# Performance work log

Measured on AMD Instinct MI355X. Metric: run time of the kernel, lower is better.

Reference implementation:

```python
import jax, jax.numpy as jnp
import numpy as np

N, E = 100000, 1600000
D_IN, H, C = 128, 4, 32
NEG_SLOPE = 0.2

def setup_inputs() -> dict:
    key = jax.random.key(0)
    ks = jax.random.split(key, 6)
    x = jax.random.normal(ks[0], (N, D_IN), dtype=jnp.float32)
    edge_index = jax.random.randint(ks[1], (2, E), 0, N, dtype=jnp.int64)
    s = 1.0 / np.sqrt(D_IN)
    W_l = jax.random.normal(ks[2], (D_IN, H * C), dtype=jnp.float32) * s
    W_r = jax.random.normal(ks[3], (D_IN, H * C), dtype=jnp.float32) * s
    att = jax.random.normal(ks[4], (H, C), dtype=jnp.float32) * (1.0 / np.sqrt(C))
    bias = jax.random.normal(ks[5], (H * C,), dtype=jnp.float32) * 0.01
    return {"x": x, "edge_index": edge_index, "W_l": W_l, "W_r": W_r, "att": att, "bias": bias}

def reference(x, edge_index, W_l, W_r, att, bias):
    # GATv2: e_ij = att . LeakyReLU(W_l x_j + W_r x_i); softmax over incoming edges of i;
    # out_i = sum_j alpha_ij * (W_l x_j); heads concatenated, then bias.
    src, dst = edge_index[0], edge_index[1]
    n = x.shape[0]
    xl = (x @ W_l).reshape(n, H, C)   # source transform (lin_l)
    xr = (x @ W_r).reshape(n, H, C)   # target transform (lin_r)
    xj = xl[src]                       # [E,H,C] gathered source feats
    xi = xr[dst]                       # [E,H,C] gathered target feats
    e = jax.nn.leaky_relu(xi + xj, NEG_SLOPE)
    score = jnp.einsum('ehc,hc->eh', e, att)          # [E,H]
    # segment softmax over destination nodes
    m = jax.ops.segment_max(score, dst, num_segments=n)  # [N,H]
    ex = jnp.exp(score - m[dst])
    denom = jax.ops.segment_sum(ex, dst, num_segments=n)  # [N,H]
    alpha = ex / (denom[dst] + 1e-16)                      # [E,H]
    out = jax.ops.segment_sum(alpha[..., None] * xj, dst, num_segments=n)  # [N,H,C]
    return out.reshape(n, H * C) + bias
```

## Files before the change

kernel.cpp:

```cpp
#include <hip/hip_runtime.h>
#include <hip/hip_bf16.h>
#include <math.h>

#define N_NODES 100000
#define E_EDGES 1600000
#define D 128
#define NEG_SLOPE 0.2f

#define BSH   8
#define NBKT  391
#define BCAP  4992
#define P1_EPB 8192

typedef __bf16 bf16x8 __attribute__((ext_vector_type(8)));
typedef float f32x4 __attribute__((ext_vector_type(4)));

__device__ __forceinline__ float bf2f(unsigned short u) {
    union { unsigned int i; float f; } x; x.i = ((unsigned int)u) << 16; return x.f;
}
__device__ __forceinline__ unsigned short f2bf(float f) {
    union { float f; unsigned int i; } x; x.f = f;
    unsigned int r = x.i + 0x7fffu + ((x.i >> 16) & 1u);
    return (unsigned short)(r >> 16);
}
__device__ __forceinline__ void unpack4(uint2 u, float* x) {
    union { unsigned int i; float f; } a, b, c, d;
    a.i = u.x << 16; b.i = u.x & 0xffff0000u;
    c.i = u.y << 16; d.i = u.y & 0xffff0000u;
    x[0] = a.f; x[1] = b.f; x[2] = c.f; x[3] = d.f;
}

__global__ void GATv2Conv_56908316672629_kernel(
    const unsigned int* ei_words, int* flags)
{
    __shared__ int cnt_edge;
    if (threadIdx.x == 0) cnt_edge = 0;
    __syncthreads();
    unsigned int w = ei_words[2 * threadIdx.x + 1];
    if (w != 0u) atomicAdd(&cnt_edge, 1);
    __syncthreads();
    if (threadIdx.x == 0) flags[0] = (cnt_edge == 0) ? 1 : 0;
}

__global__ __launch_bounds__(256) void gemm_f32_kernel(
    const float* __restrict__ X,
    const float* __restrict__ Wl,
    const float* __restrict__ Wr,
    unsigned short* __restrict__ xl, unsigned short* __restrict__ xr,
    int nblk)
{
    __shared__ unsigned short Xs[64][136];
    __shared__ unsigned short Wt[128][136];

    const int bid = blockIdx.x;
    const int sel = (bid >= nblk) ? 1 : 0;
    const float* W = sel ? Wr : Wl;
    unsigned short* out = sel ? xr : xl;
    const int rowbase = (bid - sel * nblk) * 64;
    const int tid = threadIdx.x;

    for (int c = tid; c < 4096; c += 256) {
        int k = c >> 5, n4 = (c & 31) << 2;
        float4 w = ((const float4*)(W + (size_t)k * D))[c & 31];
        Wt[n4 + 0][k] = f2bf(w.x);
        Wt[n4 + 1][k] = f2bf(w.y);
        Wt[n4 + 2][k] = f2bf(w.z);
        Wt[n4 + 3][k] = f2bf(w.w);
    }
    for (int c = tid; c < 2048; c += 256) {
        int r = c >> 5, k4 = (c & 31) << 2;
        int grow = rowbase + r;
        float4 v = make_float4(0.f, 0.f, 0.f, 0.f);
        if (grow < N_NODES) v = ((const float4*)(X + (size_t)grow * D))[c & 31];
        union { unsigned short us[4]; uint2 u2; } pk;
        pk.us[0] = f2bf(v.x); pk.us[1] = f2bf(v.y);
        pk.us[2] = f2bf(v.z); pk.us[3] = f2bf(v.w);
        *((uint2*)&Xs[r][k4]) = pk.u2;
    }
    __syncthreads();

    const int wave = tid >> 6, lane = tid & 63;
    const int mrow = lane & 15, quad = lane >> 4;

    f32x4 acc[8];
#pragma unroll
    for (int i = 0; i < 8; ++i) acc[i] = (f32x4){0.f, 0.f, 0.f, 0.f};

#pragma unroll
    for (int kk = 0; kk < 4; ++kk) {
        const int k0 = kk * 32 + quad * 8;
        bf16x8 afrag = *(const bf16x8*)&Xs[wave * 16 + mrow][k0];
#pragma unroll
        for (int n0 = 0; n0 < 8; ++n0) {
            bf16x8 bfrag = *(const bf16x8*)&Wt[n0 * 16 + mrow][k0];
            acc[n0] = __builtin_amdgcn_mfma_f32_16x16x32_bf16(afrag, bfrag, acc[n0], 0, 0, 0);
        }
    }

    const int grow0 = rowbase + wave * 16 + quad * 4;
#pragma unroll
    for (int n0 = 0; n0 < 8; ++n0) {
        int col = n0 * 16 + mrow;
#pragma unroll
        for (int r = 0; r < 4; ++r) {
            int grow = grow0 + r;
            if (grow < N_NODES) out[(size_t)grow * D + col] = f2bf(acc[n0][r]);
        }
    }
}

__global__ void zero_kernel(int* p, int n) {
    int i = blockIdx.x * 256 + threadIdx.x;
    if (i < n) p[i] = 0;
}

__device__ __forceinline__ unsigned int edge_word(const unsigned int* ei, int is64,
                                                  long long entry) {
    return is64 ? ei[2 * entry] : ei[entry];
}

__global__ __launch_bounds__(256) void bucket_scatter_kernel(
    const unsigned int* __restrict__ ei, const int* __restrict__ flags,
    int* __restrict__ bcur, unsigned int* __restrict__ pairbuf)
{
    __shared__ int h[NBKT];
    __shared__ int gbase[NBKT];

    const int tid = threadIdx.x;
    const int is64 = flags[0];
    const long long e0 = (long long)blockIdx.x * P1_EPB;
    int n = E_EDGES - (int)e0; if (n > P1_EPB) n = P1_EPB;

    for (int i = tid; i < NBKT; i += 256) h[i] = 0;
    __syncthreads();

    for (int i = tid; i < n; i += 256) {
        unsigned int s = edge_word(ei, is64, e0 + i);
        unsigned int d = edge_word(ei, is64, (long long)E_EDGES + e0 + i);
        if (d < N_NODES && s < N_NODES) atomicAdd(&h[d >> BSH], 1);
    }
    __syncthreads();

    for (int i = tid; i < NBKT; i += 256) {
        int c = h[i];
        gbase[i] = c ? atomicAdd(&bcur[i], c) : 0;
        h[i] = 0;
    }
    __syncthreads();

    for (int i = tid; i < n; i += 256) {
        unsigned int s = edge_word(ei, is64, e0 + i);
        unsigned int d = edge_word(ei, is64, (long long)E_EDGES + e0 + i);
        if (d < N_NODES && s < N_NODES) {
            int b = (int)(d >> BSH);
            int r = gbase[b] + atomicAdd(&h[b], 1);
            if (r < BCAP)
                pairbuf[(size_t)b * BCAP + r] = s | ((d & 255u) << 24);
        }
    }
}

__global__ __launch_bounds__(256) void bucket_sort_kernel(
    const int* __restrict__ bcur, unsigned int* __restrict__ pairbuf,
    int* __restrict__ rowstart, int* __restrict__ rowend)
{
    __shared__ unsigned int stage[BCAP];
    __shared__ int cnt[256];
    __shared__ int base[256];

    const int b = blockIdx.x;
    const int tid = threadIdx.x;
    int n = bcur[b]; if (n > BCAP) n = BCAP;
    unsigned int* buf = pairbuf + (size_t)b * BCAP;

    for (int i = tid; i < n; i += 256) stage[i] = buf[i];
    cnt[tid] = 0;
    __syncthreads();

    for (int i = tid; i < n; i += 256) atomicAdd(&cnt[stage[i] >> 24], 1);
    __syncthreads();

    int v = cnt[tid];
    base[tid] = v;
    __syncthreads();
    for (int off = 1; off < 256; off <<= 1) {
        int u = (tid >= off) ? base[tid - off] : 0;
        __syncthreads();
        base[tid] += u;
        __syncthreads();
    }
    const int myend = base[tid];
    const int mystart = myend - v;

    const int node = b * 256 + tid;
    if (node < N_NODES) {
        rowstart[node] = b * BCAP + mystart;
        rowend[node]   = b * BCAP + myend;
    }

    cnt[tid] = mystart;
    __syncthreads();

    for (int i = tid; i < n; i += 256) {
        unsigned int p = stage[i];
        int pos = atomicAdd(&cnt[p >> 24], 1);
        buf[pos] = p & 0x00FFFFFFu;
    }
}

__global__ __launch_bounds__(256) void aggregate_kernel(
    const unsigned short* __restrict__ xl, const unsigned short* __restrict__ xr,
    const int* __restrict__ rowstart, const int* __restrict__ rowend,
    const int* __restrict__ ssrc,
    const float* __restrict__ att, const float* __restrict__ bias,
    float* __restrict__ out)
{
    const int t = threadIdx.x & 31;
    const int node = blockIdx.x * 8 + (threadIdx.x >> 5);
    if (node >= N_NODES) return;
    const int f0 = t * 4;

    float xr4[4], att4[4];
    unpack4(*(const uint2*)&xr[(size_t)node * D + f0], xr4);
    att4[0] = att[f0]; att4[1] = att[f0 + 1];
    att4[2] = att[f0 + 2]; att4[3] = att[f0 + 3];

    const int p0 = rowstart[node];
    const int p1 = rowend[node];

    float l = 0.f;
    float acc[4] = {0.f, 0.f, 0.f, 0.f};

    int p = p0;
    for (; p + 2 <= p1; p += 2) {
        int sa = ssrc[p], sb = ssrc[p + 1];
        uint2 ua = *(const uint2*)&xl[(size_t)sa * D + f0];
        uint2 ub = *(const uint2*)&xl[(size_t)sb * D + f0];
        float xa[4], xb[4];
        unpack4(ua, xa); unpack4(ub, xb);
        float pa = 0.f, pb = 0.f;
#pragma unroll
        for (int j = 0; j < 4; ++j) {
            float va = xa[j] + xr4[j];
            float vb = xb[j] + xr4[j];
            pa = fmaf(att4[j], fmaxf(va, NEG_SLOPE * va), pa);
            pb = fmaf(att4[j], fmaxf(vb, NEG_SLOPE * vb), pb);
        }
#pragma unroll
        for (int off = 1; off < 8; off <<= 1) {
            pa += __shfl_xor(pa, off);
            pb += __shfl_xor(pb, off);
        }
        float wa = __expf(pa), wb = __expf(pb);
        l += wa + wb;
#pragma unroll
        for (int j = 0; j < 4; ++j)
            acc[j] = fmaf(wb, xb[j], fmaf(wa, xa[j], acc[j]));
    }
    if (p < p1) {
        int sa = ssrc[p];
        float xa[4];
        unpack4(*(const uint2*)&xl[(size_t)sa * D + f0], xa);
        float pa = 0.f;
#pragma unroll
        for (int j = 0; j < 4; ++j) {
            float va = xa[j] + xr4[j];
            pa = fmaf(att4[j], fmaxf(va, NEG_SLOPE * va), pa);
        }
#pragma unroll
        for (int off = 1; off < 8; off <<= 1) pa += __shfl_xor(pa, off);
        float wa = __expf(pa);
        l += wa;
#pragma unroll
        for (int j = 0; j < 4; ++j) acc[j] = fmaf(wa, xa[j], acc[j]);
    }

    const float inv = (l > 0.f) ? (1.f / l) : 0.f;
    float4 o;
    o.x = fmaf(acc[0], inv, bias[f0]);
    o.y = fmaf(acc[1], inv, bias[f0 + 1]);
    o.z = fmaf(acc[2], inv, bias[f0 + 2]);
    o.w = fmaf(acc[3], inv, bias[f0 + 3]);
    *(float4*)&out[(size_t)node * D + f0] = o;
}

extern "C" void kernel_launch(void* const* d_in, const int* in_sizes, int n_in,
                              void* d_out, int out_size, void* d_ws, size_t ws_size,
                              hipStream_t stream)
{
    const float*        X    = (const float*)d_in[0];
    const unsigned int* ei   = (const unsigned int*)d_in[1];
    const float*        Wl   = (const float*)d_in[2];
    const float*        Wr   = (const float*)d_in[3];
    const float*        att  = (const float*)d_in[4];
    const float*        bias = (const float*)d_in[5];

    char* ws = (char*)d_ws;
    size_t off = 0;
    unsigned short* xl = (unsigned short*)(ws + off); off += (size_t)N_NODES * D * 2;
    unsigned short* xr = (unsigned short*)(ws + off); off += (size_t)N_NODES * D * 2;
    unsigned int* pairbuf = (unsigned int*)(ws + off); off += (size_t)NBKT * BCAP * 4;
    int* rowstart = (int*)(ws + off); off += (size_t)N_NODES * 4;
    int* rowend   = (int*)(ws + off); off += (size_t)N_NODES * 4;
    int* bcur     = (int*)(ws + off); off += (size_t)((NBKT + 255) & ~255) * 4;
    int* flags    = (int*)(ws + off); off += 256;

    const int gb = (N_NODES + 63) / 64;
    const int p1b = (E_EDGES + P1_EPB - 1) / P1_EPB;

    GATv2Conv_56908316672629_kernel<<<1, 256, 0, stream>>>(ei, flags);

    gemm_f32_kernel<<<gb * 2, 256, 0, stream>>>(X, Wl, Wr, xl, xr, gb);

    zero_kernel<<<(NBKT + 255) / 256, 256, 0, stream>>>(bcur, NBKT);
    bucket_scatter_kernel<<<p1b, 256, 0, stream>>>(ei, flags, bcur, pairbuf);
    bucket_sort_kernel<<<NBKT, 256, 0, stream>>>(bcur, pairbuf, rowstart, rowend);

    aggregate_kernel<<<(N_NODES + 7) / 8, 256, 0, stream>>>(
        xl, xr, rowstart, rowend, (const int*)pairbuf, att, bias, (float*)d_out);
}
```

Measured before the change: 288.2 us.

## Reuse X tile for both projections, register-cache edges, pack aggregate math

Result: faster. 276.2 us (-4.2%).

```diff
diff --git a/kernel.cpp b/kernel.cpp
--- a/kernel.cpp
+++ b/kernel.cpp
@@ -11,9 +11,12 @@
 #define NBKT  391
 #define BCAP  4992
 #define P1_EPB 8192
+#define P1_TPB 512
+#define P1_EPT 16
 
 typedef __bf16 bf16x8 __attribute__((ext_vector_type(8)));
 typedef float f32x4 __attribute__((ext_vector_type(4)));
+typedef float f32x2 __attribute__((ext_vector_type(2)));
 
 __device__ __forceinline__ float bf2f(unsigned short u) {
     union { unsigned int i; float f; } x; x.i = ((unsigned int)u) << 16; return x.f;
@@ -23,11 +26,16 @@
     unsigned int r = x.i + 0x7fffu + ((x.i >> 16) & 1u);
     return (unsigned short)(r >> 16);
 }
-__device__ __forceinline__ void unpack4(uint2 u, float* x) {
+__device__ __forceinline__ void unpack4p(uint2 u, f32x2* lo, f32x2* hi) {
     union { unsigned int i; float f; } a, b, c, d;
     a.i = u.x << 16; b.i = u.x & 0xffff0000u;
     c.i = u.y << 16; d.i = u.y & 0xffff0000u;
-    x[0] = a.f; x[1] = b.f; x[2] = c.f; x[3] = d.f;
+    *lo = (f32x2){a.f, b.f}; *hi = (f32x2){c.f, d.f};
+}
+__device__ __forceinline__ f32x2 pabs(f32x2 v) {
+    union { f32x2 f; unsigned int u[2]; } x; x.f = v;
+    x.u[0] &= 0x7fffffffu; x.u[1] &= 0x7fffffffu;
+    return x.f;
 }
 
 __global__ void GATv2Conv_56908316672629_kernel(
@@ -46,27 +54,14 @@
     const float* __restrict__ X,
     const float* __restrict__ Wl,
     const float* __restrict__ Wr,
-    unsigned short* __restrict__ xl, unsigned short* __restrict__ xr,
-    int nblk)
+    unsigned short* __restrict__ xl, unsigned short* __restrict__ xr)
 {
     __shared__ unsigned short Xs[64][136];
     __shared__ unsigned short Wt[128][136];
 
-    const int bid = blockIdx.x;
-    const int sel = (bid >= nblk) ? 1 : 0;
-    const float* W = sel ? Wr : Wl;
-    unsigned short* out = sel ? xr : xl;
-    const int rowbase = (bid - sel * nblk) * 64;
+    const int rowbase = blockIdx.x * 64;
     const int tid = threadIdx.x;
 
-    for (int c = tid; c < 4096; c += 256) {
-        int k = c >> 5, n4 = (c & 31) << 2;
-        float4 w = ((const float4*)(W + (size_t)k * D))[c & 31];
-        Wt[n4 + 0][k] = f2bf(w.x);
-        Wt[n4 + 1][k] = f2bf(w.y);
-        Wt[n4 + 2][k] = f2bf(w.z);
-        Wt[n4 + 3][k] = f2bf(w.w);
-    }
     for (int c = tid; c < 2048; c += 256) {
         int r = c >> 5, k4 = (c & 31) << 2;
         int grow = rowbase + r;
@@ -77,34 +72,49 @@
         pk.us[2] = f2bf(v.z); pk.us[3] = f2bf(v.w);
         *((uint2*)&Xs[r][k4]) = pk.u2;
     }
-    __syncthreads();
 
     const int wave = tid >> 6, lane = tid & 63;
     const int mrow = lane & 15, quad = lane >> 4;
 
-    f32x4 acc[8];
-#pragma unroll
-    for (int i = 0; i < 8; ++i) acc[i] = (f32x4){0.f, 0.f, 0.f, 0.f};
-
-#pragma unroll
-    for (int kk = 0; kk < 4; ++kk) {
-        const int k0 = kk * 32 + quad * 8;
-        bf16x8 afrag = *(const bf16x8*)&Xs[wave * 16 + mrow][k0];
+    for (int sel = 0; sel < 2; ++sel) {
+        const float* W = sel ? Wr : Wl;
+        unsigned short* out = sel ? xr : xl;
+
+        if (sel) __syncthreads();
+        for (int c = tid; c < 4096; c += 256) {
+            int k = c >> 5, n4 = (c & 31) << 2;
+            float4 w = ((const float4*)(W + (size_t)k * D))[c & 31];
+            Wt[n4 + 0][k] = f2bf(w.x);
+            Wt[n4 + 1][k] = f2bf(w.y);
+            Wt[n4 + 2][k] = f2bf(w.z);
+            Wt[n4 + 3][k] = f2bf(w.w);
+        }
+        __syncthreads();
+
+        f32x4 acc[8];
+#pragma unroll
+        for (int i = 0; i < 8; ++i) acc[i] = (f32x4){0.f, 0.f, 0.f, 0.f};
+
+#pragma unroll
+        for (int kk = 0; kk < 4; ++kk) {
+            const int k0 = kk * 32 + quad * 8;
+            bf16x8 afrag = *(const bf16x8*)&Xs[wave * 16 + mrow][k0];
+#pragma unroll
+            for (int n0 = 0; n0 < 8; ++n0) {
+                bf16x8 bfrag = *(const bf16x8*)&Wt[n0 * 16 + mrow][k0];
+                acc[n0] = __builtin_amdgcn_mfma_f32_16x16x32_bf16(afrag, bfrag, acc[n0], 0, 0, 0);
+            }
+        }
+
+        const int grow0 = rowbase + wave * 16 + quad * 4;
 #pragma unroll
         for (int n0 = 0; n0 < 8; ++n0) {
-            bf16x8 bfrag = *(const bf16x8*)&Wt[n0 * 16 + mrow][k0];
-            acc[n0] = __builtin_amdgcn_mfma_f32_16x16x32_bf16(afrag, bfrag, acc[n0], 0, 0, 0);
-        }
-    }
-
-    const int grow0 = rowbase + wave * 16 + quad * 4;
-#pragma unroll
-    for (int n0 = 0; n0 < 8; ++n0) {
-        int col = n0 * 16 + mrow;
-#pragma unroll
-        for (int r = 0; r < 4; ++r) {
-            int grow = grow0 + r;
-            if (grow < N_NODES) out[(size_t)grow * D + col] = f2bf(acc[n0][r]);
+            int col = n0 * 16 + mrow;
+#pragma unroll
+            for (int r = 0; r < 4; ++r) {
+                int grow = grow0 + r;
+                if (grow < N_NODES) out[(size_t)grow * D + col] = f2bf(acc[n0][r]);
+            }
         }
     }
 }
@@ -119,7 +129,7 @@
     return is64 ? ei[2 * entry] : ei[entry];
 }
 
-__global__ __launch_bounds__(256) void bucket_scatter_kernel(
+__global__ __launch_bounds__(P1_TPB) void bucket_scatter_kernel(
     const unsigned int* __restrict__ ei, const int* __restrict__ flags,
     int* __restrict__ bcur, unsigned int* __restrict__ pairbuf)
 {
@@ -129,33 +139,43 @@
     const int tid = threadIdx.x;
     const int is64 = flags[0];
     const long long e0 = (long long)blockIdx.x * P1_EPB;
-    int n = E_EDGES - (int)e0; if (n > P1_EPB) n = P1_EPB;
-
-    for (int i = tid; i < NBKT; i += 256) h[i] = 0;
-    __syncthreads();
-
-    for (int i = tid; i < n; i += 256) {
-        unsigned int s = edge_word(ei, is64, e0 + i);
-        unsigned int d = edge_word(ei, is64, (long long)E_EDGES + e0 + i);
-        if (d < N_NODES && s < N_NODES) atomicAdd(&h[d >> BSH], 1);
-    }
-    __syncthreads();
-
-    for (int i = tid; i < NBKT; i += 256) {
+
+    unsigned int sv[P1_EPT], dv[P1_EPT];
+#pragma unroll
+    for (int j = 0; j < P1_EPT; ++j) {
+        long long e = e0 + j * P1_TPB + tid;
+        unsigned int s = 0u, d = 0xffffffffu;
+        if (e < E_EDGES) {
+            s = edge_word(ei, is64, e);
+            d = edge_word(ei, is64, (long long)E_EDGES + e);
+            if (s >= N_NODES || d >= N_NODES) d = 0xffffffffu;
+        }
+        sv[j] = s; dv[j] = d;
+    }
+
+    for (int i = tid; i < NBKT; i += P1_TPB) h[i] = 0;
+    __syncthreads();
+
+#pragma unroll
+    for (int j = 0; j < P1_EPT; ++j)
+        if (dv[j] != 0xffffffffu) atomicAdd(&h[dv[j] >> BSH], 1);
+    __syncthreads();
+
+    for (int i = tid; i < NBKT; i += P1_TPB) {
         int c = h[i];
         gbase[i] = c ? atomicAdd(&bcur[i], c) : 0;
         h[i] = 0;
     }
     __syncthreads();
 
-    for (int i = tid; i < n; i += 256) {
-        unsigned int s = edge_word(ei, is64, e0 + i);
-        unsigned int d = edge_word(ei, is64, (long long)E_EDGES + e0 + i);
-        if (d < N_NODES && s < N_NODES) {
+#pragma unroll
+    for (int j = 0; j < P1_EPT; ++j) {
+        unsigned int d = dv[j];
+        if (d != 0xffffffffu) {
             int b = (int)(d >> BSH);
             int r = gbase[b] + atomicAdd(&h[b], 1);
             if (r < BCAP)
-                pairbuf[(size_t)b * BCAP + r] = s | ((d & 255u) << 24);
+                pairbuf[(size_t)b * BCAP + r] = sv[j] | ((d & 255u) << 24);
         }
     }
 }
@@ -220,67 +240,79 @@
     if (node >= N_NODES) return;
     const int f0 = t * 4;
 
-    float xr4[4], att4[4];
-    unpack4(*(const uint2*)&xr[(size_t)node * D + f0], xr4);
-    att4[0] = att[f0]; att4[1] = att[f0 + 1];
-    att4[2] = att[f0 + 2]; att4[3] = att[f0 + 3];
+    f32x2 xr0, xr1;
+    unpack4p(*(const uint2*)&xr[(size_t)node * D + f0], &xr0, &xr1);
+    f32x2 a60 = (f32x2){0.6f * att[f0], 0.6f * att[f0 + 1]};
+    f32x2 a61 = (f32x2){0.6f * att[f0 + 2], 0.6f * att[f0 + 3]};
+    f32x2 a40 = (f32x2){0.4f * att[f0], 0.4f * att[f0 + 1]};
+    f32x2 a41 = (f32x2){0.4f * att[f0 + 2], 0.4f * att[f0 + 3]};
+
+    const uint2* xlp = (const uint2*)xl + (f0 >> 2);
 
     const int p0 = rowstart[node];
     const int p1 = rowend[node];
 
     float l = 0.f;
-    float acc[4] = {0.f, 0.f, 0.f, 0.f};
+    f32x2 acc0 = (f32x2){0.f, 0.f}, acc1 = (f32x2){0.f, 0.f};
+
+#define ESCORE(u, xa0, xa1, pe)                                   \
+    {                                                             \
+        unpack4p(u, &xa0, &xa1);                                  \
+        f32x2 v0 = xa0 + xr0, v1 = xa1 + xr1;                     \
+        f32x2 pp = v0 * a60;                                      \
+        pp += pabs(v0) * a40;                                     \
+        pp += v1 * a61;                                           \
+        pp += pabs(v1) * a41;                                     \
+        pe = pp.x + pp.y;                                         \
+    }
 
     int p = p0;
-    for (; p + 2 <= p1; p += 2) {
-        int sa = ssrc[p], sb = ssrc[p + 1];
-        uint2 ua = *(const uint2*)&xl[(size_t)sa * D + f0];
-        uint2 ub = *(const uint2*)&xl[(size_t)sb * D + f0];
-        float xa[4], xb[4];
-        unpack4(ua, xa); unpack4(ub, xb);
-        float pa = 0.f, pb = 0.f;
-#pragma unroll
-        for (int j = 0; j < 4; ++j) {
-            float va = xa[j] + xr4[j];
-            float vb = xb[j] + xr4[j];
-            pa = fmaf(att4[j], fmaxf(va, NEG_SLOPE * va), pa);
-            pb = fmaf(att4[j], fmaxf(vb, NEG_SLOPE * vb), pb);
-        }
+    for (; p + 4 <= p1; p += 4) {
+        int s0 = ssrc[p], s1 = ssrc[p + 1], s2 = ssrc[p + 2], s3 = ssrc[p + 3];
+        uint2 u0 = xlp[(size_t)s0 * 32];
+        uint2 u1 = xlp[(size_t)s1 * 32];
+        uint2 u2 = xlp[(size_t)s2 * 32];
+        uint2 u3 = xlp[(size_t)s3 * 32];
+        f32x2 xa0, xa1, xb0, xb1, xc0, xc1, xd0, xd1;
+        float e0, e1, e2, e3;
+        ESCORE(u0, xa0, xa1, e0);
+        ESCORE(u1, xb0, xb1, e1);
+        ESCORE(u2, xc0, xc1, e2);
+        ESCORE(u3, xd0, xd1, e3);
 #pragma unroll
         for (int off = 1; off < 8; off <<= 1) {
-            pa += __shfl_xor(pa, off);
-            pb += __shfl_xor(pb, off);
-        }
-        float wa = __expf(pa), wb = __expf(pb);
-        l += wa + wb;
-#pragma unroll
-        for (int j = 0; j < 4; ++j)
-            acc[j] = fmaf(wb, xb[j], fmaf(wa, xa[j], acc[j]));
-    }
-    if (p < p1) {
-        int sa = ssrc[p];
-        float xa[4];
-        unpack4(*(const uint2*)&xl[(size_t)sa * D + f0], xa);
-        float pa = 0.f;
-#pragma unroll
-        for (int j = 0; j < 4; ++j) {
-            float va = xa[j] + xr4[j];
-            pa = fmaf(att4[j], fmaxf(va, NEG_SLOPE * va), pa);
-        }
-#pragma unroll
-        for (int off = 1; off < 8; off <<= 1) pa += __shfl_xor(pa, off);
-        float wa = __expf(pa);
-        l += wa;
-#pragma unroll
-        for (int j = 0; j < 4; ++j) acc[j] = fmaf(wa, xa[j], acc[j]);
-    }
+            e0 += __shfl_xor(e0, off);
+            e1 += __shfl_xor(e1, off);
+            e2 += __shfl_xor(e2, off);
+            e3 += __shfl_xor(e3, off);
+        }
+        float w0 = __expf(e0), w1 = __expf(e1), w2 = __expf(e2), w3 = __expf(e3);
+        l += (w0 + w1) + (w2 + w3);
+        acc0 += w0 * xa0; acc1 += w0 * xa1;
+        acc0 += w1 * xb0; acc1 += w1 * xb1;
+        acc0 += w2 * xc0; acc1 += w2 * xc1;
+        acc0 += w3 * xd0; acc1 += w3 * xd1;
+    }
+    for (; p < p1; ++p) {
+        int s0 = ssrc[p];
+        uint2 u0 = xlp[(size_t)s0 * 32];
+        f32x2 xa0, xa1;
+        float e0;
+        ESCORE(u0, xa0, xa1, e0);
+#pragma unroll
+        for (int off = 1; off < 8; off <<= 1) e0 += __shfl_xor(e0, off);
+        float w0 = __expf(e0);
+        l += w0;
+        acc0 += w0 * xa0; acc1 += w0 * xa1;
+    }
+#undef ESCORE
 
     const float inv = (l > 0.f) ? (1.f / l) : 0.f;
     float4 o;
-    o.x = fmaf(acc[0], inv, bias[f0]);
-    o.y = fmaf(acc[1], inv, bias[f0 + 1]);
-    o.z = fmaf(acc[2], inv, bias[f0 + 2]);
-    o.w = fmaf(acc[3], inv, bias[f0 + 3]);
+    o.x = fmaf(acc0.x, inv, bias[f0]);
+    o.y = fmaf(acc0.y, inv, bias[f0 + 1]);
+    o.z = fmaf(acc1.x, inv, bias[f0 + 2]);
+    o.w = fmaf(acc1.y, inv, bias[f0 + 3]);
     *(float4*)&out[(size_t)node * D + f0] = o;
 }
 
@@ -310,10 +342,10 @@
 
     GATv2Conv_56908316672629_kernel<<<1, 256, 0, stream>>>(ei, flags);
 
-    gemm_f32_kernel<<<gb * 2, 256, 0, stream>>>(X, Wl, Wr, xl, xr, gb);
+    gemm_f32_kernel<<<gb, 256, 0, stream>>>(X, Wl, Wr, xl, xr);
 
     zero_kernel<<<(NBKT + 255) / 256, 256, 0, stream>>>(bcur, NBKT);
-    bucket_scatter_kernel<<<p1b, 256, 0, stream>>>(ei, flags, bcur, pairbuf);
+    bucket_scatter_kernel<<<p1b, P1_TPB, 0, stream>>>(ei, flags, bcur, pairbuf);
     bucket_sort_kernel<<<NBKT, 256, 0, stream>>>(bcur, pairbuf, rowstart, rowend);
 
     aggregate_kernel<<<(N_NODES + 7) / 8, 256, 0, stream>>>(
```
